# Kernel optimization log

Hardware: AMD Instinct MI355X
Metric: run time of the kernel (lower is better)

## Reference

```python
import jax, jax.numpy as jnp
import numpy as np

STEPS = 250
BETA = 0.02


def setup_inputs() -> dict:
    key = jax.random.key(0)
    k1, k2 = jax.random.split(key)
    reflectance_normal = jax.random.normal(k1, (8, 1024, 1024), dtype=jnp.float32)
    distribution = jax.random.normal(k2, (8, 65536), dtype=jnp.float32)
    return {"reflectance_normal": reflectance_normal, "distribution": distribution}


def reference(reflectance_normal, distribution):
    # Faithful vectorized version of ForwardDiffusionModel.forward:
    # per batch element, 250 steps of xt = sqrt(1-b)*xt + sqrt(b)*sample,
    # where sample is drawn i.i.d. uniformly (with replacement) from the
    # flattened empirical distribution values of that batch element.
    B = reflectance_normal.shape[0]
    flat = distribution.reshape(B, -1)          # [B, N]
    N = flat.shape[1]
    a = np.sqrt(1.0 - BETA).astype(np.float32)
    b = np.sqrt(BETA).astype(np.float32)
    sample_shape = reflectance_normal.shape     # [B, H, W]

    keys = jax.random.split(jax.random.key(42), STEPS)

    def step(xt, k):
        idx = jax.random.randint(k, sample_shape, 0, N)                 # [B,H,W]
        sample = jnp.take_along_axis(flat, idx.reshape(B, -1), axis=1)  # [B,H*W]
        sample = sample.reshape(sample_shape)
        return a * xt + b * sample, None

    xt, _ = jax.lax.scan(step, reflectance_normal, keys)
    return xt
```

## Files before the change

kernel.cpp:

```cpp
#include <hip/hip_runtime.h>
#include <hip/hip_fp16.h>
#include <stdint.h>

#define NDIST 65536
#define NSTEPS 250

#if __has_builtin(__builtin_rotateleft32)
#define ROTL(x, r) __builtin_rotateleft32((x), (r))
#else
#define ROTL(x, r) (((x) << (r)) | ((x) >> (32 - (r))))
#endif

#define TF_ROUND(r) { x0 += x1; x1 = ROTL(x1, r); x1 ^= x0; }

__device__ __forceinline__ uint2 threefry2x32(uint32_t ks0, uint32_t ks1, uint32_t ks2,
                                              uint32_t x0, uint32_t x1) {
  x0 += ks0; x1 += ks1;
  TF_ROUND(13) TF_ROUND(15) TF_ROUND(26) TF_ROUND(6)
  x0 += ks1; x1 += ks2 + 1u;
  TF_ROUND(17) TF_ROUND(29) TF_ROUND(16) TF_ROUND(24)
  x0 += ks2; x1 += ks0 + 2u;
  TF_ROUND(13) TF_ROUND(15) TF_ROUND(26) TF_ROUND(6)
  x0 += ks0; x1 += ks1 + 3u;
  TF_ROUND(17) TF_ROUND(29) TF_ROUND(16) TF_ROUND(24)
  x0 += ks1; x1 += ks2 + 4u;
  TF_ROUND(13) TF_ROUND(15) TF_ROUND(26) TF_ROUND(6)
  x0 += ks2; x1 += ks0 + 5u;
  return make_uint2(x0, x1);
}


__global__ void keys_kernel(uint32_t* __restrict__ ks_out) {
  const int tid = threadIdx.x;
  if (tid < NSTEPS) {
    uint2 ks = threefry2x32(0u, 42u, 0x1BD11BDAu ^ 42u, 0u, (uint32_t)tid);
    uint2 k2 = threefry2x32(ks.x, ks.y, ks.x ^ ks.y ^ 0x1BD11BDAu, 0u, 1u);
    ks_out[2 * tid]     = k2.x;
    ks_out[2 * tid + 1] = k2.y;
  }
}

#define WGL 1024
#define GL  16

__global__ __launch_bounds__(WGL, 1) void fwd_diff_v2(
    const float* __restrict__ x_init,
    const float* __restrict__ dist,
    const uint32_t* __restrict__ keysg,
    float* __restrict__ out) {
  extern __shared__ __half tab[];

  const int tid   = threadIdx.x;
  const int batch = blockIdx.x >> 6;
  const int chunk = blockIdx.x & 63;
  const uint32_t base = ((uint32_t)batch << 20) + ((uint32_t)chunk << 14);

  const float Ac = 0.9899494936611665f;
  const float Bc = 0.1414213562373095f;

  const float4* src = reinterpret_cast<const float4*>(dist + (size_t)batch * NDIST);
  for (int i = tid; i < NDIST / 4; i += WGL) {
    float4 v = src[i];
    ushort4 h;
    h.x = __half_as_ushort(__float2half(Bc * v.x));
    h.y = __half_as_ushort(__float2half(Bc * v.y));
    h.z = __half_as_ushort(__float2half(Bc * v.z));
    h.w = __half_as_ushort(__float2half(Bc * v.w));
    reinterpret_cast<ushort4*>(tab)[i] = h;
  }
  __syncthreads();

  uint32_t p[GL];
  float acc[GL];
#pragma unroll
  for (int j = 0; j < GL; ++j) {
    p[j]   = base + (uint32_t)(j * WGL) + (uint32_t)tid;
    acc[j] = x_init[p[j]];
  }

  for (int s = 0; s < NSTEPS; ++s) {
    const uint32_t kx = keysg[2 * s];
    const uint32_t ky = keysg[2 * s + 1];
    const uint32_t kz = kx ^ ky ^ 0x1BD11BDAu;

    uint32_t idx[GL];
#pragma unroll
    for (int j = 0; j < GL; ++j) {
      uint2 r = threefry2x32(kx, ky, kz, 0u, p[j]);
      idx[j] = r.y & 0xFFFFu;
    }
#pragma unroll
    for (int j = 0; j < GL; ++j) {
      acc[j] = fmaf(Ac, acc[j], __half2float(tab[idx[j]]));
    }
  }

#pragma unroll
  for (int j = 0; j < GL; ++j) out[p[j]] = acc[j];
}

#define GF9 8

__global__ __launch_bounds__(WGL, 1) void fwd_diff_full(
    const float* __restrict__ x_init,
    const float* __restrict__ dist,
    float* __restrict__ out) {
  extern __shared__ char smem[];
  __half*   tab9 = reinterpret_cast<__half*>(smem);
  uint32_t* keys = reinterpret_cast<uint32_t*>(smem + 131072);

  const int tid   = threadIdx.x;
  const int batch = blockIdx.x >> 7;
  const int chunk = blockIdx.x & 127;
  const uint32_t base = ((uint32_t)batch << 20) + ((uint32_t)chunk << 13);

  const float Ac = 0.9899494936611665f;
  const float Bc = 0.1414213562373095f;

  const float4* src = reinterpret_cast<const float4*>(dist + (size_t)batch * NDIST);
  for (int i = tid; i < NDIST / 4; i += WGL) {
    float4 v = src[i];
    ushort4 h;
    h.x = __half_as_ushort(__float2half(Bc * v.x));
    h.y = __half_as_ushort(__float2half(Bc * v.y));
    h.z = __half_as_ushort(__float2half(Bc * v.z));
    h.w = __half_as_ushort(__float2half(Bc * v.w));
    reinterpret_cast<ushort4*>(tab9)[i] = h;
  }
  if (tid < NSTEPS) {
    uint2 ks = threefry2x32(0u, 42u, 0x1BD11BDAu ^ 42u, 0u, (uint32_t)tid);
    uint2 k2 = threefry2x32(ks.x, ks.y, ks.x ^ ks.y ^ 0x1BD11BDAu, 0u, 1u);
    keys[2 * tid]     = k2.x;
    keys[2 * tid + 1] = k2.y;
  }
  __syncthreads();

  uint32_t p[GF9];
  float acc[GF9];
#pragma unroll
  for (int j = 0; j < GF9; ++j) {
    p[j]   = base + (uint32_t)(j * WGL) + (uint32_t)tid;
    acc[j] = x_init[p[j]];
  }

  for (int s = 0; s < NSTEPS; ++s) {
    uint32_t kx = keys[2 * s];
    uint32_t ky = keys[2 * s + 1];
    kx = (uint32_t)__builtin_amdgcn_readfirstlane((int)kx);
    ky = (uint32_t)__builtin_amdgcn_readfirstlane((int)ky);
    const uint32_t kz = kx ^ ky ^ 0x1BD11BDAu;
#pragma unroll
    for (int j = 0; j < GF9; ++j) {
      uint2 r = threefry2x32(kx, ky, kz, 0u, p[j]);
      uint32_t idx = r.y & 0xFFFFu;
      acc[j] = fmaf(Ac, acc[j], __half2float(tab9[idx]));
    }
  }

#pragma unroll
  for (int j = 0; j < GF9; ++j) out[p[j]] = acc[j];
}

extern "C" void kernel_launch(void* const* d_in, const int* in_sizes, int n_in,
                              void* d_out, int out_size, void* d_ws, size_t ws_size,
                              hipStream_t stream) {
  const float* x_init = (const float*)d_in[0];
  const float* dist   = (const float*)d_in[1];
  if (n_in >= 2 && in_sizes[0] == 8 * NDIST) {
    x_init = (const float*)d_in[1];
    dist   = (const float*)d_in[0];
  }
  float* out = (float*)d_out;
  uint32_t* keysg = (uint32_t*)d_ws;

  const int smem_v2 = 131072;

  hipError_t st = hipFuncSetAttribute(
      reinterpret_cast<const void*>(fwd_diff_v2),
      hipFuncAttributeMaxDynamicSharedMemorySize, smem_v2);
  int max_blocks = 0;
  if (st == hipSuccess) {
    st = hipOccupancyMaxActiveBlocksPerMultiprocessor(
        &max_blocks, reinterpret_cast<const void*>(fwd_diff_v2), WGL, smem_v2);
  }

  if (st == hipSuccess && max_blocks >= 1 && ws_size >= 2 * NSTEPS * sizeof(uint32_t)) {
    keys_kernel<<<dim3(1), dim3(256), 0, stream>>>(keysg);
    fwd_diff_v2<<<dim3(512), dim3(WGL), smem_v2, stream>>>(x_init, dist, keysg, out);
  } else {
    const int smem_v1 = 131072 + 2048;
    (void)hipFuncSetAttribute(reinterpret_cast<const void*>(fwd_diff_full),
                              hipFuncAttributeMaxDynamicSharedMemorySize, smem_v1);
    fwd_diff_full<<<dim3(1024), dim3(WGL), smem_v1, stream>>>(x_init, dist, out);
  }
}
```

Baseline: 3.543 ms.

## Software-pipeline threefry index generation with LDS gathers, halve per-thread elements

```diff
diff --git a/kernel.cpp b/kernel.cpp
--- a/kernel.cpp
+++ b/kernel.cpp
@@ -27,6 +27,21 @@
   TF_ROUND(13) TF_ROUND(15) TF_ROUND(26) TF_ROUND(6)
   x0 += ks2; x1 += ks0 + 5u;
   return make_uint2(x0, x1);
+}
+
+__device__ __forceinline__ uint32_t threefry2x32_y(uint32_t ks0, uint32_t ks1, uint32_t ks2,
+                                                   uint32_t x0, uint32_t x1) {
+  x0 += ks0; x1 += ks1;
+  TF_ROUND(13) TF_ROUND(15) TF_ROUND(26) TF_ROUND(6)
+  x0 += ks1; x1 += ks2 + 1u;
+  TF_ROUND(17) TF_ROUND(29) TF_ROUND(16) TF_ROUND(24)
+  x0 += ks2; x1 += ks0 + 2u;
+  TF_ROUND(13) TF_ROUND(15) TF_ROUND(26) TF_ROUND(6)
+  x0 += ks0; x1 += ks1 + 3u;
+  TF_ROUND(17) TF_ROUND(29) TF_ROUND(16) TF_ROUND(24)
+  x0 += ks1; x1 += ks2 + 4u;
+  TF_ROUND(13) TF_ROUND(15) TF_ROUND(26) TF_ROUND(6)
+  return x1 + ks0 + 5u;
 }
 
 
@@ -41,9 +56,9 @@
 }
 
 #define WGL 1024
-#define GL  16
-
-__global__ __launch_bounds__(WGL, 1) void fwd_diff_v2(
+#define GL  8
+
+__global__ __launch_bounds__(WGL, 1) void fwd_diff_v3(
     const float* __restrict__ x_init,
     const float* __restrict__ dist,
     const uint32_t* __restrict__ keysg,
@@ -51,9 +66,9 @@
   extern __shared__ __half tab[];
 
   const int tid   = threadIdx.x;
-  const int batch = blockIdx.x >> 6;
-  const int chunk = blockIdx.x & 63;
-  const uint32_t base = ((uint32_t)batch << 20) + ((uint32_t)chunk << 14);
+  const int batch = blockIdx.x >> 7;
+  const int chunk = blockIdx.x & 127;
+  const uint32_t base = ((uint32_t)batch << 20) + ((uint32_t)chunk << 13);
 
   const float Ac = 0.9899494936611665f;
   const float Bc = 0.1414213562373095f;
@@ -78,21 +93,34 @@
     acc[j] = x_init[p[j]];
   }
 
+  uint32_t idx[GL];
+  {
+    const uint32_t kx = keysg[0];
+    const uint32_t ky = keysg[1];
+    const uint32_t kz = kx ^ ky ^ 0x1BD11BDAu;
+#pragma unroll
+    for (int j = 0; j < GL; ++j)
+      idx[j] = threefry2x32_y(kx, ky, kz, 0u, p[j]) & 0xFFFFu;
+  }
+
   for (int s = 0; s < NSTEPS; ++s) {
-    const uint32_t kx = keysg[2 * s];
-    const uint32_t ky = keysg[2 * s + 1];
-    const uint32_t kz = kx ^ ky ^ 0x1BD11BDAu;
-
-    uint32_t idx[GL];
-#pragma unroll
-    for (int j = 0; j < GL; ++j) {
-      uint2 r = threefry2x32(kx, ky, kz, 0u, p[j]);
-      idx[j] = r.y & 0xFFFFu;
+    float sv[GL];
+#pragma unroll
+    for (int j = 0; j < GL; ++j)
+      sv[j] = __half2float(tab[idx[j]]);
+
+    if (s + 1 < NSTEPS) {
+      const uint32_t kx = keysg[2 * (s + 1)];
+      const uint32_t ky = keysg[2 * (s + 1) + 1];
+      const uint32_t kz = kx ^ ky ^ 0x1BD11BDAu;
+#pragma unroll
+      for (int j = 0; j < GL; ++j)
+        idx[j] = threefry2x32_y(kx, ky, kz, 0u, p[j]) & 0xFFFFu;
     }
-#pragma unroll
-    for (int j = 0; j < GL; ++j) {
-      acc[j] = fmaf(Ac, acc[j], __half2float(tab[idx[j]]));
-    }
+
+#pragma unroll
+    for (int j = 0; j < GL; ++j)
+      acc[j] = fmaf(Ac, acc[j], sv[j]);
   }
 
 #pragma unroll
@@ -152,8 +180,8 @@
 #pragma unroll
     for (int j = 0; j < GF9; ++j) {
       uint2 r = threefry2x32(kx, ky, kz, 0u, p[j]);
-      uint32_t idx = r.y & 0xFFFFu;
-      acc[j] = fmaf(Ac, acc[j], __half2float(tab9[idx]));
+      uint32_t idx9 = r.y & 0xFFFFu;
+      acc[j] = fmaf(Ac, acc[j], __half2float(tab9[idx9]));
     }
   }
 
@@ -173,20 +201,20 @@
   float* out = (float*)d_out;
   uint32_t* keysg = (uint32_t*)d_ws;
 
-  const int smem_v2 = 131072;
+  const int smem_v3 = 131072;
 
   hipError_t st = hipFuncSetAttribute(
-      reinterpret_cast<const void*>(fwd_diff_v2),
-      hipFuncAttributeMaxDynamicSharedMemorySize, smem_v2);
+      reinterpret_cast<const void*>(fwd_diff_v3),
+      hipFuncAttributeMaxDynamicSharedMemorySize, smem_v3);
   int max_blocks = 0;
   if (st == hipSuccess) {
     st = hipOccupancyMaxActiveBlocksPerMultiprocessor(
-        &max_blocks, reinterpret_cast<const void*>(fwd_diff_v2), WGL, smem_v2);
+        &max_blocks, reinterpret_cast<const void*>(fwd_diff_v3), WGL, smem_v3);
   }
 
   if (st == hipSuccess && max_blocks >= 1 && ws_size >= 2 * NSTEPS * sizeof(uint32_t)) {
     keys_kernel<<<dim3(1), dim3(256), 0, stream>>>(keysg);
-    fwd_diff_v2<<<dim3(512), dim3(WGL), smem_v2, stream>>>(x_init, dist, keysg, out);
+    fwd_diff_v3<<<dim3(1024), dim3(WGL), smem_v3, stream>>>(x_init, dist, keysg, out);
   } else {
     const int smem_v1 = 131072 + 2048;
     (void)hipFuncSetAttribute(reinterpret_cast<const void*>(fwd_diff_full),
```

Result: no change. 3.591 ms (+1.3%).
